# Kernel tuning notes

Hardware: AMD Instinct MI355X
Metric: run time of the kernel (lower is better)

The kernel has to match this reference:

```python
import jax, jax.numpy as jnp
import numpy as np

HEADS = 16
HEAD_DIM = 64
DIM = 1024
WH, WW = 32, 32
ROPE_DIM = 32  # = HEAD_DIM // 2
ROPE_BASE = 10000
EPS = 1e-6


def _rope_cache():
    # theta: [ROPE_DIM//2]
    theta = 1.0 / (ROPE_BASE ** (jnp.arange(0, ROPE_DIM, 2, dtype=jnp.float32)[: ROPE_DIM // 2] / ROPE_DIM))
    n = WH * WW
    idx = jnp.arange(n, dtype=jnp.float32)
    x_pos = idx % WW
    y_pos = idx // WW
    freqs = jnp.concatenate([x_pos[:, None] * theta[None, :], y_pos[:, None] * theta[None, :]], axis=-1)  # [n, ROPE_DIM]
    return jnp.cos(freqs), jnp.sin(freqs)


def _apply_rope(x, cos, sin):
    # x: [b, h, n, HEAD_DIM] -> pairs [b, h, n, ROPE_DIM, 2]
    xf = x.astype(jnp.float32).reshape(*x.shape[:-1], -1, 2)
    x0, x1 = xf[..., 0], xf[..., 1]
    c = cos[None, None, :, :]
    s = sin[None, None, :, :]
    out = jnp.stack([x0 * c - x1 * s, x1 * c + x0 * s], axis=-1)
    return out.reshape(*x.shape).astype(x.dtype)


def setup_inputs() -> dict:
    key = jax.random.key(0)
    ks = jax.random.split(key, 5)
    b, n = 16, WH * WW
    inner = HEADS * HEAD_DIM
    return {
        "x": jax.random.normal(ks[0], (b, n, DIM), dtype=jnp.float32),
        "t": jax.random.normal(ks[1], (b, DIM), dtype=jnp.float32),
        "norm_w": jnp.ones((DIM,), dtype=jnp.float32),
        "mod_w": jax.random.normal(ks[2], (2 * DIM, DIM), dtype=jnp.float32) * (DIM ** -0.5),
        "qkv_w": jax.random.normal(ks[3], (3 * inner, DIM), dtype=jnp.float32) * (DIM ** -0.5),
        "wo_w": jax.random.normal(ks[4], (DIM, inner), dtype=jnp.float32) * (inner ** -0.5),
    }


def reference(x, t, norm_w, mod_w, qkv_w, wo_w):
    b, n, dim = x.shape
    scale = HEAD_DIM ** -0.5

    # Modulated RMSNorm
    xf = x.astype(jnp.float32)
    xn = (xf * jax.lax.rsqrt(jnp.mean(xf * xf, axis=-1, keepdims=True) + EPS)).astype(x.dtype) * norm_w
    mod = t @ mod_w.T  # [b, 2*dim]
    sc, sh = mod[:, :dim], mod[:, dim:]
    h = xn * (1.0 + sc[:, None, :]) + sh[:, None, :]

    # QKV projection; rearrange 'b n (h d) -> b h n d' with d = 3*HEAD_DIM, THEN chunk
    qkv = h @ qkv_w.T  # [b, n, 3*inner]
    qkv = qkv.reshape(b, n, HEADS, 3 * HEAD_DIM).transpose(0, 2, 1, 3)  # [b, H, n, 3*hd]
    q, k, v = qkv[..., :HEAD_DIM], qkv[..., HEAD_DIM:2 * HEAD_DIM], qkv[..., 2 * HEAD_DIM:]

    # 2D axial RoPE on q, k
    cos, sin = _rope_cache()
    q = _apply_rope(q, cos, sin)
    k = _apply_rope(k, cos, sin)

    # SDPA (non-causal)
    attn = jax.nn.softmax(jnp.einsum('bhqd,bhkd->bhqk', q * scale, k), axis=-1)
    out = jnp.einsum('bhqk,bhkd->bhqd', attn, v)  # [b, H, n, hd]
    out = out.transpose(0, 2, 1, 3).reshape(b, n, HEADS * HEAD_DIM)
    return out @ wo_w.T
```

## Files before the change

kernel.cpp:

```cpp
#include <hip/hip_runtime.h>
#include <stdint.h>

typedef __bf16    bf16x8 __attribute__((ext_vector_type(8)));
typedef float     f32x4  __attribute__((ext_vector_type(4)));
typedef _Float16  f16;
typedef _Float16  f16x2  __attribute__((ext_vector_type(2)));
typedef _Float16  f16x4  __attribute__((ext_vector_type(4)));
typedef _Float16  f16x8  __attribute__((ext_vector_type(8)));

#define DEV __device__ __forceinline__

DEV ushort f2bf(float f) {
  union { float f; uint32_t u; } v; v.f = f;
  uint32_t u = v.u;
  return (ushort)((u + 0x7fffu + ((u >> 16) & 1u)) >> 16);
}

DEV f16x2 cvt_pkrtz(float a, float b) {
  return __builtin_bit_cast(f16x2, __builtin_amdgcn_cvt_pkrtz(a, b));
}

DEV void async16(const void* g, void* l) {
  __builtin_amdgcn_global_load_lds(
      (__attribute__((address_space(1))) void*)(uintptr_t)g,
      (__attribute__((address_space(3))) void*)(uint32_t)(uintptr_t)l,
      16, 0, 0);
}

__global__ __launch_bounds__(256)
void prep_kernel(const float* __restrict__ t, const float* __restrict__ mw,
                 float* __restrict__ mod,
                 const float* __restrict__ qkvw, ushort* __restrict__ wqk,
                 ushort* __restrict__ wv,
                 const float* __restrict__ wow, ushort* __restrict__ wowb) {
  const int id = blockIdx.x;
  const int tid = threadIdx.x;
  if (id < 2048) {
    const int j = id;
    const int w = tid >> 6, lane = tid & 63;
    float wr[16];
#pragma unroll
    for (int i = 0; i < 16; ++i) wr[i] = mw[(size_t)j * 1024 + lane + i * 64];
#pragma unroll
    for (int bb = 0; bb < 4; ++bb) {
      int b = w * 4 + bb;
      float s = 0.f;
#pragma unroll
      for (int i = 0; i < 16; ++i) s += wr[i] * t[b * 1024 + lane + i * 64];
#pragma unroll
      for (int m = 32; m >= 1; m >>= 1) s += __shfl_xor(s, m, 64);
      if (lane == 0) mod[b * 2048 + j] = s;
    }
  } else if (id < 5120) {
    const int j = id - 2048;
    uint32_t hd = (uint32_t)j / 192u;
    uint32_t rem = (uint32_t)j - hd * 192u;
    ushort* dst = (rem < 128u) ? (wqk + (size_t)(hd * 128u + rem) * 1024)
                               : (wv + (size_t)(hd * 64u + (rem - 128u)) * 1024);
    float4 v = ((const float4*)(qkvw + (size_t)j * 1024))[tid];
    ushort4 o;
    o.x = f2bf(v.x); o.y = f2bf(v.y); o.z = f2bf(v.z); o.w = f2bf(v.w);
    ((ushort4*)dst)[tid] = o;
  } else {
    const int i = (id - 5120) * 256 + tid;
    float4 v = ((const float4*)wow)[i];
    ushort4 o;
    o.x = f2bf(v.x); o.y = f2bf(v.y); o.z = f2bf(v.z); o.w = f2bf(v.w);
    ((ushort4*)wowb)[i] = o;
  }
}

__global__ __launch_bounds__(256)
void rms_mod_kernel(const float* __restrict__ x, const float* __restrict__ nw,
                    const float* __restrict__ mod, ushort* __restrict__ h) {
  int row = blockIdx.x;
  int b = row >> 10;
  int tid = threadIdx.x;
  const float4 xv = *(const float4*)(x + (size_t)row * 1024 + tid * 4);
  float ss = xv.x * xv.x + xv.y * xv.y + xv.z * xv.z + xv.w * xv.w;
#pragma unroll
  for (int m = 32; m >= 1; m >>= 1) ss += __shfl_xor(ss, m, 64);
  __shared__ float red[4];
  int w = tid >> 6, lane = tid & 63;
  if (lane == 0) red[w] = ss;
  __syncthreads();
  float tot = red[0] + red[1] + red[2] + red[3];
  float rn = rsqrtf(tot * (1.f / 1024.f) + 1e-6f);
  float4 wv = *(const float4*)(nw + tid * 4);
  float4 sc = *(const float4*)(mod + (size_t)b * 2048 + tid * 4);
  float4 sh = *(const float4*)(mod + (size_t)b * 2048 + 1024 + tid * 4);
  ushort4 o;
  o.x = f2bf(xv.x * rn * wv.x * (1.f + sc.x) + sh.x);
  o.y = f2bf(xv.y * rn * wv.y * (1.f + sc.y) + sh.y);
  o.z = f2bf(xv.z * rn * wv.z * (1.f + sc.z) + sh.z);
  o.w = f2bf(xv.w * rn * wv.w * (1.f + sc.w) + sh.w);
  *(ushort4*)(h + (size_t)row * 1024 + tid * 4) = o;
}

__global__ __launch_bounds__(512, 2)
void gemm_qkv_kernel(const ushort* __restrict__ hbuf, const ushort* __restrict__ wqk,
                     const ushort* __restrict__ wvw,
                     f16* __restrict__ qb, f16* __restrict__ kb,
                     f16* __restrict__ vtb) {
  __shared__ ushort smem[65536];
  const int id0 = blockIdx.x;
  const int id = (id0 & 7) * 96 + (id0 >> 3);
  int mode, m0, n0;
  const ushort *A, *B;
  if (id < 512) {
    mode = 1; m0 = (id >> 3) * 256; n0 = (id & 7) * 256; A = hbuf; B = wqk;
  } else {
    const int i2 = id - 512;
    mode = 2; n0 = (i2 >> 2) * 256; m0 = (i2 & 3) * 256; A = wvw; B = hbuf;
  }
  const int tid = threadIdx.x;
  const int w = tid >> 6, lane = tid & 63, quad = lane >> 4, l15 = lane & 15;
  const int wm = w >> 2, wn = w & 3;

  const int srow = tid >> 3;
  const int sch  = (tid & 7) ^ (srow & 7);
  const int soff = srow * 1024 + sch * 8;
  const ushort* const Abase = A + (size_t)m0 * 1024;
  const ushort* const Bbase = B + (size_t)n0 * 1024;
  ushort* const As0 = smem;
  ushort* const Bs0 = smem + 32768;
  const int sdst = tid * 8;

#define STG_A(d, t, h) do { \
    async16(Abase + (h) * 131072 + soff + (t) * 64,          As0 + (d) * 16384 + (h) * 8192 + sdst); \
    async16(Abase + (h) * 131072 + 65536 + soff + (t) * 64,  As0 + (d) * 16384 + (h) * 8192 + 4096 + sdst); } while (0)
#define STG_B(d, t, h) do { \
    async16(Bbase + (h) * 131072 + soff + (t) * 64,          Bs0 + (d) * 16384 + (h) * 8192 + sdst); \
    async16(Bbase + (h) * 131072 + 65536 + soff + (t) * 64,  Bs0 + (d) * 16384 + (h) * 8192 + 4096 + sdst); } while (0)

  int aoff[2], boff[2];
#pragma unroll
  for (int kk = 0; kk < 2; ++kk) {
    const int swz = (((kk * 4 + quad) ^ (l15 & 7)) * 8);
    aoff[kk] = (wm * 128 + l15) * 64 + swz;
    boff[kk] = (wn * 64 + l15) * 64 + swz;
  }

  const f32x4 fzero = {0.f, 0.f, 0.f, 0.f};
  f32x4 acc[8][4];
#pragma unroll
  for (int a = 0; a < 8; ++a)
#pragma unroll
    for (int b = 0; b < 4; ++b) acc[a][b] = fzero;

  STG_A(0, 0, 0); STG_A(0, 0, 1); STG_B(0, 0, 0); STG_B(0, 0, 1);
  asm volatile("s_waitcnt vmcnt(0)" ::: "memory");
  __builtin_amdgcn_s_barrier();

  bf16x8 af[4][2];
  bf16x8 bfv[2][2];
#pragma unroll 2
  for (int t = 0; t < 16; ++t) {
    const int cur = t & 1, nxt = cur ^ 1;
    const int tn = (t < 15) ? t + 1 : 15;
    const ushort* Asc = As0 + cur * 16384;
    const ushort* Bsc = Bs0 + cur * 16384;

#pragma unroll
    for (int mf = 0; mf < 4; ++mf)
#pragma unroll
      for (int kk = 0; kk < 2; ++kk)
        af[mf][kk] = *(const bf16x8*)(Asc + mf * 1024 + aoff[kk]);
#pragma unroll
    for (int nf = 0; nf < 2; ++nf)
#pragma unroll
      for (int kk = 0; kk < 2; ++kk)
        bfv[nf][kk] = *(const bf16x8*)(Bsc + nf * 1024 + boff[kk]);
    STG_A(nxt, tn, 0);
    __builtin_amdgcn_s_barrier();
    __builtin_amdgcn_s_setprio(1);
#pragma unroll
    for (int mf = 0; mf < 4; ++mf)
#pragma unroll
      for (int nf = 0; nf < 2; ++nf)
#pragma unroll
        for (int kk = 0; kk < 2; ++kk)
          acc[mf][nf] = __builtin_amdgcn_mfma_f32_16x16x32_bf16(
              af[mf][kk], bfv[nf][kk], acc[mf][nf], 0, 0, 0);
    __builtin_amdgcn_s_setprio(0);
    __builtin_amdgcn_s_barrier();

#pragma unroll
    for (int mf = 0; mf < 4; ++mf)
#pragma unroll
      for (int kk = 0; kk < 2; ++kk)
        af[mf][kk] = *(const bf16x8*)(Asc + (4 + mf) * 1024 + aoff[kk]);
    STG_A(nxt, tn, 1);
    __builtin_amdgcn_s_barrier();
    __builtin_amdgcn_s_setprio(1);
#pragma unroll
    for (int mf = 0; mf < 4; ++mf)
#pragma unroll
      for (int nf = 0; nf < 2; ++nf)
#pragma unroll
        for (int kk = 0; kk < 2; ++kk)
          acc[4 + mf][nf] = __builtin_amdgcn_mfma_f32_16x16x32_bf16(
              af[mf][kk], bfv[nf][kk], acc[4 + mf][nf], 0, 0, 0);
    __builtin_amdgcn_s_setprio(0);
    __builtin_amdgcn_s_barrier();

#pragma unroll
    for (int nf = 0; nf < 2; ++nf)
#pragma unroll
      for (int kk = 0; kk < 2; ++kk)
        bfv[nf][kk] = *(const bf16x8*)(Bsc + (2 + nf) * 1024 + boff[kk]);
    STG_B(nxt, tn, 0);
    __builtin_amdgcn_s_barrier();
    __builtin_amdgcn_s_setprio(1);
#pragma unroll
    for (int mf = 0; mf < 4; ++mf)
#pragma unroll
      for (int nf = 0; nf < 2; ++nf)
#pragma unroll
        for (int kk = 0; kk < 2; ++kk)
          acc[4 + mf][2 + nf] = __builtin_amdgcn_mfma_f32_16x16x32_bf16(
              af[mf][kk], bfv[nf][kk], acc[4 + mf][2 + nf], 0, 0, 0);
    __builtin_amdgcn_s_setprio(0);
    __builtin_amdgcn_s_barrier();

#pragma unroll
    for (int mf = 0; mf < 4; ++mf)
#pragma unroll
      for (int kk = 0; kk < 2; ++kk)
        af[mf][kk] = *(const bf16x8*)(Asc + mf * 1024 + aoff[kk]);
    STG_B(nxt, tn, 1);
    __builtin_amdgcn_s_barrier();
    __builtin_amdgcn_s_setprio(1);
#pragma unroll
    for (int mf = 0; mf < 4; ++mf)
#pragma unroll
      for (int nf = 0; nf < 2; ++nf)
#pragma unroll
        for (int kk = 0; kk < 2; ++kk)
          acc[mf][2 + nf] = __builtin_amdgcn_mfma_f32_16x16x32_bf16(
              af[mf][kk], bfv[nf][kk], acc[mf][2 + nf], 0, 0, 0);
    __builtin_amdgcn_s_setprio(0);
    asm volatile("s_waitcnt vmcnt(0)" ::: "memory");
    __builtin_amdgcn_s_barrier();
  }
#undef STG_A
#undef STG_B

  ushort* eps = smem + w * 8192;
#pragma unroll
  for (int mf = 0; mf < 8; ++mf)
#pragma unroll
    for (int nf = 0; nf < 4; ++nf)
#pragma unroll
      for (int r = 0; r < 4; ++r) {
        const int row_loc = mf * 16 + quad * 4 + r;
        const int col = nf * 16 + l15;
        const int ch = (col >> 3) ^ (row_loc & 7);
        union { f16 h; ushort u; } cv;
        cv.h = (f16)acc[mf][nf][r];
        eps[row_loc * 64 + ch * 8 + (col & 7)] = cv.u;
      }

  const int ch = lane & 7;
  const int rbase = lane >> 3;
  const int gcol = n0 + wn * 64;
  if (mode == 1) {
    const int hd = gcol >> 7, part = (gcol >> 6) & 1;
    const float QS = part ? 1.f : 0.125f * 1.44269504f;
    f16* const outp = part ? kb : qb;
    float th[4];
#pragma unroll
    for (int t2 = 0; t2 < 4; ++t2)
      th[t2] = __expf(-(float)((ch * 4 + t2) & 15) * 0.5756462732485114f);
#pragma unroll
    for (int i = 0; i < 16; ++i) {
      const int row_loc = i * 8 + rbase;
      union { uint4 u4; f16 h[8]; } uv;
      uv.u4 = *(const uint4*)(eps + row_loc * 64 + ((ch ^ (row_loc & 7)) * 8));
      const int m = m0 + wm * 128 + row_loc;
      const int n = m & 1023;
      const float xpos = (float)(n & 31), ypos = (float)(n >> 5);
#pragma unroll
      for (int t2 = 0; t2 < 4; ++t2) {
        const int p = ch * 4 + t2;
        const float pos = (p < 16) ? xpos : ypos;
        float sn, cs;
        __sincosf(pos * th[t2], &sn, &cs);
        const float x0 = (float)uv.h[2 * t2], x1 = (float)uv.h[2 * t2 + 1];
        f16x2 ro = cvt_pkrtz((x0 * cs - x1 * sn) * QS, (x1 * cs + x0 * sn) * QS);
        uv.h[2 * t2] = ro[0];
        uv.h[2 * t2 + 1] = ro[1];
      }
      f16* dst = outp + (((size_t)((m >> 10) * 16 + hd) * 1024 + n) * 64 + ch * 8);
      *(uint4*)dst = uv.u4;
    }
  } else {
    const int b = gcol >> 10, tb = gcol & 1023;
#pragma unroll
    for (int i = 0; i < 16; ++i) {
      const int row_loc = i * 8 + rbase;
      uint4 v = *(const uint4*)(eps + row_loc * 64 + ((ch ^ (row_loc & 7)) * 8));
      if (i & 1) { unsigned t0 = v.x, t1 = v.y; v.x = v.z; v.y = v.w; v.z = t0; v.w = t1; }
      const int m = m0 + wm * 128 + row_loc;
      f16* dst = vtb + ((size_t)(b * 1024 + m) * 1024 + tb + ch * 8);
      *(uint4*)dst = v;
    }
  }
}

__global__ __launch_bounds__(256, 3)
void gemm_wo_kernel(const ushort* __restrict__ A, const ushort* __restrict__ B,
                    float* __restrict__ outf) {
  __shared__ ushort smem[8192];
  ushort* As = smem;
  ushort* Bs = smem + 4096;
  const int K = 1024;
  const int m0 = blockIdx.y * 128, n0 = blockIdx.x * 128;
  const int tid = threadIdx.x;
  const int w = tid >> 6, lane = tid & 63, quad = lane >> 4, l15 = lane & 15;
  const int wm = (w >> 1) * 64, wn = (w & 1) * 64;
  const f32x4 fzero = {0.f, 0.f, 0.f, 0.f};
  f32x4 acc[4][4];
#pragma unroll
  for (int a = 0; a < 4; ++a)
#pragma unroll
    for (int b = 0; b < 4; ++b) acc[a][b] = fzero;

  const int s0 = tid, s1 = 256 + tid;
  const int r0 = s0 >> 2, c0 = (s0 & 3) ^ ((r0 >> 1) & 3);
  const int r1 = s1 >> 2, c1 = (s1 & 3) ^ ((r1 >> 1) & 3);
  const int b0 = m0 >> 10, nb = m0 & 1023;
  const size_t Abase = (size_t)b0 * 16 * 1024 * 64;
  const ushort* Ag0 = A + Abase + (size_t)(nb + r0) * 64 + c0 * 8;
  const ushort* Ag1 = A + Abase + (size_t)(nb + r1) * 64 + c1 * 8;
  const ushort* Bg0 = B + (size_t)(n0 + r0) * K + c0 * 8;
  const ushort* Bg1 = B + (size_t)(n0 + r1) * K + c1 * 8;

  for (int kt = 0; kt < K; kt += 32) {
    const size_t ka = (size_t)(kt >> 6) * 65536 + (size_t)(kt & 63);
    async16(Ag0 + ka, As + s0 * 8);
    async16(Ag1 + ka, As + s1 * 8);
    async16(Bg0 + kt, Bs + s0 * 8);
    async16(Bg1 + kt, Bs + s1 * 8);
    __syncthreads();
    bf16x8 af[4], bfr[4];
#pragma unroll
    for (int tm = 0; tm < 4; ++tm) {
      int r = wm + tm * 16 + l15;
      int cs = quad ^ ((r >> 1) & 3);
      af[tm] = *(const bf16x8*)(As + (r * 4 + cs) * 8);
    }
#pragma unroll
    for (int tn = 0; tn < 4; ++tn) {
      int r = wn + tn * 16 + l15;
      int cs = quad ^ ((r >> 1) & 3);
      bfr[tn] = *(const bf16x8*)(Bs + (r * 4 + cs) * 8);
    }
#pragma unroll
    for (int tm = 0; tm < 4; ++tm)
#pragma unroll
      for (int tn = 0; tn < 4; ++tn)
        acc[tm][tn] = __builtin_amdgcn_mfma_f32_16x16x32_bf16(af[tm], bfr[tn],
                                                              acc[tm][tn], 0, 0, 0);
    __syncthreads();
  }

#pragma unroll
  for (int tm = 0; tm < 4; ++tm)
#pragma unroll
    for (int tn = 0; tn < 4; ++tn) {
      int col = n0 + wn + tn * 16 + l15;
#pragma unroll
      for (int r = 0; r < 4; ++r) {
        int row = m0 + wm + tm * 16 + quad * 4 + r;
        outf[(size_t)row * 1024 + col] = acc[tm][tn][r];
      }
    }
}

__global__ __launch_bounds__(256, 2)
void attn_kernel(const f16* __restrict__ qbuf, const f16* __restrict__ kbuf,
                 const f16* __restrict__ vtbuf, ushort* __restrict__ aout) {
  __shared__ f16 Ks[2][128 * 64];
  __shared__ f16 Vs[2][64 * 128];

  const int id = blockIdx.x;
  const int xcd = id & 7, j = id >> 3;
  const int bh = xcd * 32 + (j >> 3);
  const int q0 = (j & 7) * 128;
  const f16* Qg = qbuf + (size_t)bh * 1024 * 64;
  const f16* Kg = kbuf + (size_t)bh * 1024 * 64;
  const f16* Vg = vtbuf + (size_t)bh * 64 * 1024;
  const int tid = threadIdx.x;
  const int w = tid >> 6, lane = tid & 63, quad = lane >> 4, l15 = lane & 15;
  const f32x4 fzero = {0.f, 0.f, 0.f, 0.f};

  f16x8 qf[2][2];
#pragma unroll
  for (int qs = 0; qs < 2; ++qs)
#pragma unroll
    for (int dc = 0; dc < 2; ++dc)
      qf[qs][dc] = *(const f16x8*)(Qg + (size_t)(q0 + w * 32 + qs * 16 + l15) * 64 +
                                   dc * 32 + quad * 8);

  f32x4 oacc[2][4];
#pragma unroll
  for (int qs = 0; qs < 2; ++qs)
#pragma unroll
    for (int ds = 0; ds < 4; ++ds) oacc[qs][ds] = fzero;
  float mrun[2] = {-1e30f, -1e30f}, lrun[2] = {0.f, 0.f};

#pragma unroll
  for (int i = 0; i < 4; ++i) {
    int u = i * 256 + tid, r = u >> 3, c = u & 7;
    async16(Kg + (size_t)r * 64 + (c ^ (r & 7)) * 8, &Ks[0][u * 8]);
  }
#pragma unroll
  for (int i = 0; i < 4; ++i) {
    int u = i * 256 + tid, r = u >> 4, c = u & 15;
    async16(Vg + (size_t)r * 1024 + (c ^ (r & 15)) * 8, &Vs[0][u * 8]);
  }
  __syncthreads();

#pragma unroll 2
  for (int kt = 0; kt < 1024; kt += 128) {
    const int cur = (kt >> 7) & 1;
    if (kt + 128 < 1024) {
      const int nkt = kt + 128;
#pragma unroll
      for (int i = 0; i < 4; ++i) {
        int u = i * 256 + tid, r = u >> 3, c = u & 7;
        async16(Kg + (size_t)(nkt + r) * 64 + (c ^ (r & 7)) * 8, &Ks[cur ^ 1][u * 8]);
      }
#pragma unroll
      for (int i = 0; i < 4; ++i) {
        int u = i * 256 + tid, r = u >> 4, c = u & 15;
        async16(Vg + (size_t)r * 1024 + nkt + (c ^ (r & 15)) * 8, &Vs[cur ^ 1][u * 8]);
      }
    }
    const f16* Ksc = Ks[cur];
    const f16* Vsc = Vs[cur];

    f32x4 sacc[2][8];
#pragma unroll
    for (int qs = 0; qs < 2; ++qs)
#pragma unroll
      for (int ks = 0; ks < 8; ++ks) sacc[qs][ks] = fzero;
#pragma unroll
    for (int ks = 0; ks < 8; ++ks) {
#pragma unroll
      for (int dc = 0; dc < 2; ++dc) {
        int row = ks * 16 + l15;
        int ch = (dc * 4 + quad) ^ (row & 7);
        f16x8 kf = *(const f16x8*)(Ksc + row * 64 + ch * 8);
        sacc[0][ks] = __builtin_amdgcn_mfma_f32_16x16x32_f16(kf, qf[0][dc], sacc[0][ks], 0, 0, 0);
        sacc[1][ks] = __builtin_amdgcn_mfma_f32_16x16x32_f16(kf, qf[1][dc], sacc[1][ks], 0, 0, 0);
      }
    }

    f16x4 pf[2][8];
#pragma unroll
    for (int qs = 0; qs < 2; ++qs) {
      const float* sv = (const float*)&sacc[qs][0];
      float mx = fmaxf(sv[0], sv[1]);
#pragma unroll
      for (int k = 2; k < 32; k += 2)
        mx = fmaxf(fmaxf(mx, sv[k]), sv[k + 1]);
      mx = fmaxf(mx, __shfl_xor(mx, 16, 64));
      mx = fmaxf(mx, __shfl_xor(mx, 32, 64));
      if (__any(mx - mrun[qs] > 8.f)) {
        float mnew = fmaxf(mrun[qs], mx);
        float alpha = __builtin_amdgcn_exp2f(mrun[qs] - mnew);
        mrun[qs] = mnew;
        lrun[qs] *= alpha;
        float ar[4];
#pragma unroll
        for (int r = 0; r < 4; ++r) ar[r] = __shfl(alpha, quad * 4 + r, 64);
#pragma unroll
        for (int ds = 0; ds < 4; ++ds)
#pragma unroll
          for (int r = 0; r < 4; ++r) oacc[qs][ds][r] *= ar[r];
      }
      const float mnew = mrun[qs];
      float rs = 0.f;
#pragma unroll
      for (int ks = 0; ks < 8; ++ks) {
        float p0 = __builtin_amdgcn_exp2f(sacc[qs][ks][0] - mnew);
        float p1 = __builtin_amdgcn_exp2f(sacc[qs][ks][1] - mnew);
        float p2 = __builtin_amdgcn_exp2f(sacc[qs][ks][2] - mnew);
        float p3 = __builtin_amdgcn_exp2f(sacc[qs][ks][3] - mnew);
        rs += (p0 + p1) + (p2 + p3);
        union { f16x4 v; f16x2 h[2]; } pu;
        pu.h[0] = cvt_pkrtz(p0, p1);
        pu.h[1] = cvt_pkrtz(p2, p3);
        pf[qs][ks] = pu.v;
      }
      rs += __shfl_xor(rs, 16, 64);
      rs += __shfl_xor(rs, 32, 64);
      lrun[qs] += rs;
    }

#pragma unroll
    for (int ks = 0; ks < 8; ++ks) {
#pragma unroll
      for (int ds = 0; ds < 4; ++ds) {
        int row = ds * 16 + l15;
        int c16 = ks * 2 + (quad >> 1);
        int half = (quad & 1) ^ ((l15 >> 3) & 1);
        f16x4 vf = *(const f16x4*)(Vsc + row * 128 + ((c16 ^ (row & 15)) * 8) + half * 4);
        oacc[0][ds] = __builtin_amdgcn_mfma_f32_16x16x16f16(pf[0][ks], vf, oacc[0][ds], 0, 0, 0);
        oacc[1][ds] = __builtin_amdgcn_mfma_f32_16x16x16f16(pf[1][ks], vf, oacc[1][ds], 0, 0, 0);
      }
    }
    __syncthreads();
  }

  ushort* eps = (ushort*)&Ks[0][0] + w * 2048;
#pragma unroll
  for (int qs = 0; qs < 2; ++qs) {
    float linv[4];
#pragma unroll
    for (int r = 0; r < 4; ++r)
      linv[r] = __builtin_amdgcn_rcpf(__shfl(lrun[qs], quad * 4 + r, 64));
#pragma unroll
    for (int ds = 0; ds < 4; ++ds)
#pragma unroll
      for (int r = 0; r < 4; ++r) {
        int row_loc = qs * 16 + quad * 4 + r;
        int col = ds * 16 + l15;
        int ch = (col >> 3) ^ (row_loc & 7);
        eps[row_loc * 64 + ch * 8 + (col & 7)] = f2bf(oacc[qs][ds][r] * linv[r]);
      }
  }
  __syncthreads();
  const size_t obase = ((size_t)bh * 1024 + q0 + w * 32) * 64;
#pragma unroll
  for (int i = 0; i < 4; ++i) {
    int row_loc = i * 8 + (lane >> 3);
    int ch = lane & 7;
    uint4 v = *(const uint4*)(eps + row_loc * 64 + ((ch ^ (row_loc & 7)) * 8));
    *(uint4*)(aout + obase + row_loc * 64 + ch * 8) = v;
  }
}

extern "C" void kernel_launch(void* const* d_in, const int* in_sizes, int n_in,
                              void* d_out, int out_size, void* d_ws, size_t ws_size,
                              hipStream_t stream) {
  const float* x    = (const float*)d_in[0];
  const float* t    = (const float*)d_in[1];
  const float* nw   = (const float*)d_in[2];
  const float* mw   = (const float*)d_in[3];
  const float* qkvw = (const float*)d_in[4];
  const float* wow  = (const float*)d_in[5];
  float* out = (float*)d_out;
  char* ws = (char*)d_ws;

  float*  modbuf  = (float*)(ws);
  ushort* hbuf    = (ushort*)(ws + 131072);
  ushort* wqk_b   = (ushort*)(ws + 33685504);
  ushort* wv_b    = (ushort*)(ws + 37879808);
  ushort* wow_b   = (ushort*)(ws + 39976960);
  f16*    qbuf    = (f16*)(ws + 42074112);
  f16*    kbuf    = (f16*)(ws + 75628544);
  f16*    vtbuf   = (f16*)(ws + 109182976);
  ushort* abuf    = (ushort*)(ws + 142737408);

  prep_kernel<<<dim3(6144), dim3(256), 0, stream>>>(
      t, mw, modbuf, qkvw, wqk_b, wv_b, wow, wow_b);
  rms_mod_kernel<<<dim3(16384), dim3(256), 0, stream>>>(x, nw, modbuf, hbuf);
  gemm_qkv_kernel<<<dim3(768), dim3(512), 0, stream>>>(
      hbuf, wqk_b, wv_b, qbuf, kbuf, vtbuf);
  attn_kernel<<<dim3(2048), dim3(256), 0, stream>>>(qbuf, kbuf, vtbuf, abuf);
  gemm_wo_kernel<<<dim3(8, 128), dim3(256), 0, stream>>>(abuf, wow_b, out);
}
```

Measured before the change: 406.0 us.

## Retile output GEMM to 256x256 pipelined blocks and simplify QKV GEMM schedule

The output projection GEMM moves from 128x128 tiles with a single-buffered 32-wide K loop to 256x256 tiles with 512 threads, double-buffered 64-wide K stages and XCD-aware block ordering, mirroring the QKV GEMM design. The QKV GEMM main loop is reduced from four barrier-separated phases to two: all next-stage loads are issued up front and all four B fragments are held in registers. The aim is more data reuse per block and fewer barriers. In exchange the kernels use more registers and LDS, and the output GEMM now launches only 256 blocks.

```diff
diff --git a/kernel.cpp b/kernel.cpp
--- a/kernel.cpp
+++ b/kernel.cpp
@@ -153,7 +153,7 @@
   __builtin_amdgcn_s_barrier();
 
   bf16x8 af[4][2];
-  bf16x8 bfv[2][2];
+  bf16x8 bfp[4][2];
 #pragma unroll 2
   for (int t = 0; t < 16; ++t) {
     const int cur = t & 1, nxt = cur ^ 1;
@@ -161,27 +161,28 @@
     const ushort* Asc = As0 + cur * 16384;
     const ushort* Bsc = Bs0 + cur * 16384;
 
+    STG_A(nxt, tn, 0); STG_A(nxt, tn, 1);
+    STG_B(nxt, tn, 0); STG_B(nxt, tn, 1);
+#pragma unroll
+    for (int nf = 0; nf < 4; ++nf)
+#pragma unroll
+      for (int kk = 0; kk < 2; ++kk)
+        bfp[nf][kk] = *(const bf16x8*)(Bsc + nf * 1024 + boff[kk]);
 #pragma unroll
     for (int mf = 0; mf < 4; ++mf)
 #pragma unroll
       for (int kk = 0; kk < 2; ++kk)
         af[mf][kk] = *(const bf16x8*)(Asc + mf * 1024 + aoff[kk]);
-#pragma unroll
-    for (int nf = 0; nf < 2; ++nf)
-#pragma unroll
-      for (int kk = 0; kk < 2; ++kk)
-        bfv[nf][kk] = *(const bf16x8*)(Bsc + nf * 1024 + boff[kk]);
-    STG_A(nxt, tn, 0);
     __builtin_amdgcn_s_barrier();
     __builtin_amdgcn_s_setprio(1);
 #pragma unroll
     for (int mf = 0; mf < 4; ++mf)
 #pragma unroll
-      for (int nf = 0; nf < 2; ++nf)
+      for (int nf = 0; nf < 4; ++nf)
 #pragma unroll
         for (int kk = 0; kk < 2; ++kk)
           acc[mf][nf] = __builtin_amdgcn_mfma_f32_16x16x32_bf16(
-              af[mf][kk], bfv[nf][kk], acc[mf][nf], 0, 0, 0);
+              af[mf][kk], bfp[nf][kk], acc[mf][nf], 0, 0, 0);
     __builtin_amdgcn_s_setprio(0);
     __builtin_amdgcn_s_barrier();
 
@@ -190,55 +191,16 @@
 #pragma unroll
       for (int kk = 0; kk < 2; ++kk)
         af[mf][kk] = *(const bf16x8*)(Asc + (4 + mf) * 1024 + aoff[kk]);
-    STG_A(nxt, tn, 1);
     __builtin_amdgcn_s_barrier();
     __builtin_amdgcn_s_setprio(1);
 #pragma unroll
     for (int mf = 0; mf < 4; ++mf)
 #pragma unroll
-      for (int nf = 0; nf < 2; ++nf)
+      for (int nf = 0; nf < 4; ++nf)
 #pragma unroll
         for (int kk = 0; kk < 2; ++kk)
           acc[4 + mf][nf] = __builtin_amdgcn_mfma_f32_16x16x32_bf16(
-              af[mf][kk], bfv[nf][kk], acc[4 + mf][nf], 0, 0, 0);
-    __builtin_amdgcn_s_setprio(0);
-    __builtin_amdgcn_s_barrier();
-
-#pragma unroll
-    for (int nf = 0; nf < 2; ++nf)
-#pragma unroll
-      for (int kk = 0; kk < 2; ++kk)
-        bfv[nf][kk] = *(const bf16x8*)(Bsc + (2 + nf) * 1024 + boff[kk]);
-    STG_B(nxt, tn, 0);
-    __builtin_amdgcn_s_barrier();
-    __builtin_amdgcn_s_setprio(1);
-#pragma unroll
-    for (int mf = 0; mf < 4; ++mf)
-#pragma unroll
-      for (int nf = 0; nf < 2; ++nf)
-#pragma unroll
-        for (int kk = 0; kk < 2; ++kk)
-          acc[4 + mf][2 + nf] = __builtin_amdgcn_mfma_f32_16x16x32_bf16(
-              af[mf][kk], bfv[nf][kk], acc[4 + mf][2 + nf], 0, 0, 0);
-    __builtin_amdgcn_s_setprio(0);
-    __builtin_amdgcn_s_barrier();
-
-#pragma unroll
-    for (int mf = 0; mf < 4; ++mf)
-#pragma unroll
-      for (int kk = 0; kk < 2; ++kk)
-        af[mf][kk] = *(const bf16x8*)(Asc + mf * 1024 + aoff[kk]);
-    STG_B(nxt, tn, 1);
-    __builtin_amdgcn_s_barrier();
-    __builtin_amdgcn_s_setprio(1);
-#pragma unroll
-    for (int mf = 0; mf < 4; ++mf)
-#pragma unroll
-      for (int nf = 0; nf < 2; ++nf)
-#pragma unroll
-        for (int kk = 0; kk < 2; ++kk)
-          acc[mf][2 + nf] = __builtin_amdgcn_mfma_f32_16x16x32_bf16(
-              af[mf][kk], bfv[nf][kk], acc[mf][2 + nf], 0, 0, 0);
+              af[mf][kk], bfp[nf][kk], acc[4 + mf][nf], 0, 0, 0);
     __builtin_amdgcn_s_setprio(0);
     asm volatile("s_waitcnt vmcnt(0)" ::: "memory");
     __builtin_amdgcn_s_barrier();
@@ -308,72 +270,118 @@
   }
 }
 
-__global__ __launch_bounds__(256, 3)
+__global__ __launch_bounds__(512, 2)
 void gemm_wo_kernel(const ushort* __restrict__ A, const ushort* __restrict__ B,
                     float* __restrict__ outf) {
-  __shared__ ushort smem[8192];
-  ushort* As = smem;
-  ushort* Bs = smem + 4096;
-  const int K = 1024;
-  const int m0 = blockIdx.y * 128, n0 = blockIdx.x * 128;
+  __shared__ ushort smem[65536];
+  const int id0 = blockIdx.x;
+  const int id = (id0 & 7) * 32 + (id0 >> 3);
+  const int m0 = (id >> 2) * 256, n0 = (id & 3) * 256;
   const int tid = threadIdx.x;
   const int w = tid >> 6, lane = tid & 63, quad = lane >> 4, l15 = lane & 15;
-  const int wm = (w >> 1) * 64, wn = (w & 1) * 64;
+  const int wm = w >> 2, wn = w & 3;
+
+  const int srow = tid >> 3;
+  const int sch  = (tid & 7) ^ (srow & 7);
+  const int soff = srow * 1024 + sch * 8;
+  const int b0 = m0 >> 10, nb = m0 & 1023;
+  const ushort* const Abase = A + (size_t)b0 * 16 * 65536 + (size_t)nb * 64;
+  const ushort* const Bbase = B + (size_t)n0 * 1024;
+  ushort* const As0 = smem;
+  ushort* const Bs0 = smem + 32768;
+  const int sdst = tid * 8;
+
+#define STG_A(d, t, h) do { \
+    async16(Abase + (size_t)(t) * 65536 + ((h) * 128 + srow) * 64 + sch * 8,      As0 + (d) * 16384 + (h) * 8192 + sdst); \
+    async16(Abase + (size_t)(t) * 65536 + ((h) * 128 + 64 + srow) * 64 + sch * 8, As0 + (d) * 16384 + (h) * 8192 + 4096 + sdst); } while (0)
+#define STG_B(d, t, h) do { \
+    async16(Bbase + (h) * 131072 + soff + (t) * 64,          Bs0 + (d) * 16384 + (h) * 8192 + sdst); \
+    async16(Bbase + (h) * 131072 + 65536 + soff + (t) * 64,  Bs0 + (d) * 16384 + (h) * 8192 + 4096 + sdst); } while (0)
+
+  int aoff[2], boff[2];
+#pragma unroll
+  for (int kk = 0; kk < 2; ++kk) {
+    const int swz = (((kk * 4 + quad) ^ (l15 & 7)) * 8);
+    aoff[kk] = (wm * 128 + l15) * 64 + swz;
+    boff[kk] = (wn * 64 + l15) * 64 + swz;
+  }
+
   const f32x4 fzero = {0.f, 0.f, 0.f, 0.f};
-  f32x4 acc[4][4];
-#pragma unroll
-  for (int a = 0; a < 4; ++a)
+  f32x4 acc[8][4];
+#pragma unroll
+  for (int a = 0; a < 8; ++a)
 #pragma unroll
     for (int b = 0; b < 4; ++b) acc[a][b] = fzero;
 
-  const int s0 = tid, s1 = 256 + tid;
-  const int r0 = s0 >> 2, c0 = (s0 & 3) ^ ((r0 >> 1) & 3);
-  const int r1 = s1 >> 2, c1 = (s1 & 3) ^ ((r1 >> 1) & 3);
-  const int b0 = m0 >> 10, nb = m0 & 1023;
-  const size_t Abase = (size_t)b0 * 16 * 1024 * 64;
-  const ushort* Ag0 = A + Abase + (size_t)(nb + r0) * 64 + c0 * 8;
-  const ushort* Ag1 = A + Abase + (size_t)(nb + r1) * 64 + c1 * 8;
-  const ushort* Bg0 = B + (size_t)(n0 + r0) * K + c0 * 8;
-  const ushort* Bg1 = B + (size_t)(n0 + r1) * K + c1 * 8;
-
-  for (int kt = 0; kt < K; kt += 32) {
-    const size_t ka = (size_t)(kt >> 6) * 65536 + (size_t)(kt & 63);
-    async16(Ag0 + ka, As + s0 * 8);
-    async16(Ag1 + ka, As + s1 * 8);
-    async16(Bg0 + kt, Bs + s0 * 8);
-    async16(Bg1 + kt, Bs + s1 * 8);
-    __syncthreads();
-    bf16x8 af[4], bfr[4];
-#pragma unroll
-    for (int tm = 0; tm < 4; ++tm) {
-      int r = wm + tm * 16 + l15;
-      int cs = quad ^ ((r >> 1) & 3);
-      af[tm] = *(const bf16x8*)(As + (r * 4 + cs) * 8);
-    }
-#pragma unroll
-    for (int tn = 0; tn < 4; ++tn) {
-      int r = wn + tn * 16 + l15;
-      int cs = quad ^ ((r >> 1) & 3);
-      bfr[tn] = *(const bf16x8*)(Bs + (r * 4 + cs) * 8);
-    }
-#pragma unroll
-    for (int tm = 0; tm < 4; ++tm)
-#pragma unroll
-      for (int tn = 0; tn < 4; ++tn)
-        acc[tm][tn] = __builtin_amdgcn_mfma_f32_16x16x32_bf16(af[tm], bfr[tn],
-                                                              acc[tm][tn], 0, 0, 0);
-    __syncthreads();
-  }
-
-#pragma unroll
-  for (int tm = 0; tm < 4; ++tm)
-#pragma unroll
-    for (int tn = 0; tn < 4; ++tn) {
-      int col = n0 + wn + tn * 16 + l15;
+  STG_A(0, 0, 0); STG_A(0, 0, 1); STG_B(0, 0, 0); STG_B(0, 0, 1);
+  asm volatile("s_waitcnt vmcnt(0)" ::: "memory");
+  __builtin_amdgcn_s_barrier();
+
+  bf16x8 af[4][2];
+  bf16x8 bfp[4][2];
+#pragma unroll 2
+  for (int t = 0; t < 16; ++t) {
+    const int cur = t & 1, nxt = cur ^ 1;
+    const int tn = (t < 15) ? t + 1 : 15;
+    const ushort* Asc = As0 + cur * 16384;
+    const ushort* Bsc = Bs0 + cur * 16384;
+
+    STG_A(nxt, tn, 0); STG_A(nxt, tn, 1);
+    STG_B(nxt, tn, 0); STG_B(nxt, tn, 1);
+#pragma unroll
+    for (int nf = 0; nf < 4; ++nf)
+#pragma unroll
+      for (int kk = 0; kk < 2; ++kk)
+        bfp[nf][kk] = *(const bf16x8*)(Bsc + nf * 1024 + boff[kk]);
+#pragma unroll
+    for (int mf = 0; mf < 4; ++mf)
+#pragma unroll
+      for (int kk = 0; kk < 2; ++kk)
+        af[mf][kk] = *(const bf16x8*)(Asc + mf * 1024 + aoff[kk]);
+    __builtin_amdgcn_s_barrier();
+    __builtin_amdgcn_s_setprio(1);
+#pragma unroll
+    for (int mf = 0; mf < 4; ++mf)
+#pragma unroll
+      for (int nf = 0; nf < 4; ++nf)
+#pragma unroll
+        for (int kk = 0; kk < 2; ++kk)
+          acc[mf][nf] = __builtin_amdgcn_mfma_f32_16x16x32_bf16(
+              af[mf][kk], bfp[nf][kk], acc[mf][nf], 0, 0, 0);
+    __builtin_amdgcn_s_setprio(0);
+    __builtin_amdgcn_s_barrier();
+
+#pragma unroll
+    for (int mf = 0; mf < 4; ++mf)
+#pragma unroll
+      for (int kk = 0; kk < 2; ++kk)
+        af[mf][kk] = *(const bf16x8*)(Asc + (4 + mf) * 1024 + aoff[kk]);
+    __builtin_amdgcn_s_barrier();
+    __builtin_amdgcn_s_setprio(1);
+#pragma unroll
+    for (int mf = 0; mf < 4; ++mf)
+#pragma unroll
+      for (int nf = 0; nf < 4; ++nf)
+#pragma unroll
+        for (int kk = 0; kk < 2; ++kk)
+          acc[4 + mf][nf] = __builtin_amdgcn_mfma_f32_16x16x32_bf16(
+              af[mf][kk], bfp[nf][kk], acc[4 + mf][nf], 0, 0, 0);
+    __builtin_amdgcn_s_setprio(0);
+    asm volatile("s_waitcnt vmcnt(0)" ::: "memory");
+    __builtin_amdgcn_s_barrier();
+  }
+#undef STG_A
+#undef STG_B
+
+#pragma unroll
+  for (int mf = 0; mf < 8; ++mf)
+#pragma unroll
+    for (int nf = 0; nf < 4; ++nf) {
+      const int col = n0 + wn * 64 + nf * 16 + l15;
 #pragma unroll
       for (int r = 0; r < 4; ++r) {
-        int row = m0 + wm + tm * 16 + quad * 4 + r;
-        outf[(size_t)row * 1024 + col] = acc[tm][tn][r];
+        const int row = m0 + wm * 128 + mf * 16 + quad * 4 + r;
+        outf[(size_t)row * 1024 + col] = acc[mf][nf][r];
       }
     }
 }
@@ -571,5 +579,5 @@
   gemm_qkv_kernel<<<dim3(768), dim3(512), 0, stream>>>(
       hbuf, wqk_b, wv_b, qbuf, kbuf, vtbuf);
   attn_kernel<<<dim3(2048), dim3(256), 0, stream>>>(qbuf, kbuf, vtbuf, abuf);
-  gemm_wo_kernel<<<dim3(8, 128), dim3(256), 0, stream>>>(abuf, wow_b, out);
-}
+  gemm_wo_kernel<<<dim3(256), dim3(512), 0, stream>>>(abuf, wow_b, out);
+}
```

New measurement: 391.4 us. 3.6% less time.
